# Optimization experiments

Hardware: AMD Instinct MI355X
Metric: run time of the kernel (lower is better)

Reference implementation:

```python
import jax, jax.numpy as jnp
import numpy as np

V = 100000      # item vocab
N1, N2, N3 = 100000, 20000, 5000
EMB = 128       # embedding_dim == hidden_dim
H, Dh = 8, 16   # num_heads, per-head dim (H*Dh == EMB)
NEG_SLOPE = 0.2


def setup_inputs() -> dict:
    key = jax.random.key(0)
    ks = jax.random.split(key, 32)
    ki = iter(range(32))
    def nrm(shape, scale=0.1):
        return jax.random.normal(ks[next(ki)], shape, dtype=jnp.float32) * scale
    def ridx(n, hi):
        return jax.random.randint(ks[next(ki)], (n,), 0, hi, dtype=jnp.int32)
    inp = {}
    # graph structure
    inp['item_ids'] = ridx(N1, V)
    inp['seq1_src'] = ridx(600000, N1); inp['seq1_dst'] = ridx(600000, N1)
    inp['seq2_src'] = ridx(120000, N2); inp['seq2_dst'] = ridx(120000, N2)
    inp['seq3_src'] = ridx(30000, N3);  inp['seq3_dst'] = ridx(30000, N3)
    inp['up1_src']   = ridx(200000, N1); inp['up1_dst']   = ridx(200000, N2)
    inp['down1_src'] = ridx(200000, N2); inp['down1_dst'] = ridx(200000, N1)
    inp['up2_src']   = ridx(60000, N2);  inp['up2_dst']   = ridx(60000, N3)
    inp['down2_src'] = ridx(60000, N3);  inp['down2_dst'] = ridx(60000, N2)
    # parameters: 7 GATConvs in order [seq1, seq2, seq3, up1, down1, up2, down2]
    inp['item_emb'] = nrm((V, EMB), 1.0)
    inp['fc_w']   = nrm((7, EMB, H * Dh))   # DGL fc (bias=False)
    inp['attn_l'] = nrm((7, H, Dh))
    inp['attn_r'] = nrm((7, H, Dh))
    inp['conv_b'] = nrm((7, H * Dh))        # GATConv bias
    # 3 readout MLPs: Linear(hid,hid)->ReLU->Linear(hid,emb)
    inp['r_w1'] = nrm((3, EMB, EMB)); inp['r_b1'] = nrm((3, EMB))
    inp['r_w2'] = nrm((3, EMB, EMB)); inp['r_b2'] = nrm((3, EMB))
    inp['gran_w'] = jnp.ones((3,), dtype=jnp.float32)
    return inp


def gat(h_src, h_dst, src, dst, W, al, ar, b, residual):
    """DGL GATConv (eval mode, no dropout, no activation)."""
    Ns, Nd = h_src.shape[0], h_dst.shape[0]
    fs = (h_src @ W).reshape(Ns, H, Dh)   # [Ns,H,Dh]
    fd = (h_dst @ W).reshape(Nd, H, Dh)
    el = jnp.sum(fs * al, axis=-1)        # [Ns,H]
    er = jnp.sum(fd * ar, axis=-1)        # [Nd,H]
    e = jax.nn.leaky_relu(el[src] + er[dst], NEG_SLOPE)   # [E,H]
    m = jax.ops.segment_max(e, dst, num_segments=Nd)      # edge-softmax per dst
    ez = jnp.exp(e - m[dst])
    denom = jax.ops.segment_sum(ez, dst, num_segments=Nd)
    alpha = ez / denom[dst]                                # [E,H]
    msg = alpha[:, :, None] * fs[src]                      # [E,H,Dh]
    out = jax.ops.segment_sum(msg, dst, num_segments=Nd)   # [Nd,H,Dh]
    if residual:  # in_feats == H*Dh -> identity residual
        out = out + h_dst.reshape(Nd, H, Dh)
    out = out + b.reshape(1, H, Dh)
    return out.reshape(Nd, H * Dh)


def reference(item_emb, fc_w, attn_l, attn_r, conv_b,
              r_w1, r_b1, r_w2, r_b2, gran_w,
              item_ids, seq1_src, seq1_dst, seq2_src, seq2_dst,
              seq3_src, seq3_dst, up1_src, up1_dst, down1_src, down1_dst,
              up2_src, up2_dst, down2_src, down2_dst):
    h1 = item_emb[item_ids]                           # gran_1 from embedding lookup
    h2 = jnp.zeros((N2, EMB), dtype=item_emb.dtype)   # gran_2/3 init to zeros
    h3 = jnp.zeros((N3, EMB), dtype=item_emb.dtype)
    def g(i, hs, hd, s, d, res):
        return gat(hs, hd, s, d, fc_w[i], attn_l[i], attn_r[i], conv_b[i], res)
    out1 = g(0, h1, h1, seq1_src, seq1_dst, True) + g(4, h2, h1, down1_src, down1_dst, False)
    out2 = (g(1, h2, h2, seq2_src, seq2_dst, True)
            + g(3, h1, h2, up1_src, up1_dst, False)
            + g(6, h3, h2, down2_src, down2_dst, False))
    out3 = g(2, h3, h3, seq3_src, seq3_dst, True) + g(5, h2, h3, up2_src, up2_dst, False)
    reprs = []
    for k, x in enumerate((out1, out2, out3)):
        r = jax.nn.relu(x @ r_w1[k] + r_b1[k]) @ r_w2[k] + r_b2[k]
        reprs.append(jnp.mean(r, axis=0))             # session readout mean
    stack = jnp.stack(reprs, axis=0)                  # [3, EMB]
    weights = jax.nn.softmax(gran_w)
    fused = jnp.sum(stack * weights[:, None], axis=0) # [EMB]
    return fused, stack, weights
```

## Files before the change

### kernel.cpp

```cpp
#include <hip/hip_runtime.h>
#include <math.h>

#define N1 100000
#define N2 20000
#define EMB 128
#define NH 8
#define TILE 64
#define LPAD 132

static constexpr float NEG = 0.2f;

__global__ __launch_bounds__(256) void k_feat64(
    const float* __restrict__ item_emb, const int* __restrict__ item_ids,
    const float* __restrict__ fc_w, const float* __restrict__ attn_l,
    const float* __restrict__ attn_r,
    float* __restrict__ h1, float* __restrict__ fs0, float* __restrict__ fs3,
    float* __restrict__ el0, float* __restrict__ er0, float* __restrict__ el3)
{
    __shared__ float xs[TILE][LPAD];

    const int tid = threadIdx.x;
    const int nbase = blockIdx.x * TILE;

    #pragma unroll
    for (int r = 0; r < 8; ++r) {
        int f4 = r * 256 + tid;
        int t  = f4 >> 5;
        int c4 = f4 & 31;
        int node = nbase + t;
        if (node < N1) {
            int row = item_ids[node];
            float4 v = ((const float4*)(item_emb + (size_t)row * EMB))[c4];
            ((float4*)&xs[t][0])[c4] = v;
            ((float4*)(h1 + (size_t)node * EMB))[c4] = v;
        }
    }
    __syncthreads();

    const int cg = tid & 31;
    const int rg = tid >> 5;
    const int j0 = cg * 4;
    const float* W0 = fc_w + j0;
    const float* W3 = fc_w + 3 * EMB * EMB + j0;

    float a0[8][4], a3[8][4];
    #pragma unroll
    for (int r = 0; r < 8; ++r)
        #pragma unroll
        for (int c = 0; c < 4; ++c) { a0[r][c] = 0.f; a3[r][c] = 0.f; }

    for (int k = 0; k < EMB; k += 4) {
        float w0v[4][4], w3v[4][4];
        #pragma unroll
        for (int kk = 0; kk < 4; ++kk) {
            float4 t0 = *((const float4*)(W0 + (size_t)(k + kk) * EMB));
            float4 t3 = *((const float4*)(W3 + (size_t)(k + kk) * EMB));
            w0v[kk][0] = t0.x; w0v[kk][1] = t0.y; w0v[kk][2] = t0.z; w0v[kk][3] = t0.w;
            w3v[kk][0] = t3.x; w3v[kk][1] = t3.y; w3v[kk][2] = t3.z; w3v[kk][3] = t3.w;
        }
        #pragma unroll
        for (int r = 0; r < 8; ++r) {
            float4 x = *((const float4*)&xs[rg * 8 + r][k]);
            #pragma unroll
            for (int c = 0; c < 4; ++c) {
                a0[r][c] = fmaf(x.x, w0v[0][c], a0[r][c]);
                a0[r][c] = fmaf(x.y, w0v[1][c], a0[r][c]);
                a0[r][c] = fmaf(x.z, w0v[2][c], a0[r][c]);
                a0[r][c] = fmaf(x.w, w0v[3][c], a0[r][c]);
                a3[r][c] = fmaf(x.x, w3v[0][c], a3[r][c]);
                a3[r][c] = fmaf(x.y, w3v[1][c], a3[r][c]);
                a3[r][c] = fmaf(x.z, w3v[2][c], a3[r][c]);
                a3[r][c] = fmaf(x.w, w3v[3][c], a3[r][c]);
            }
        }
    }

    #pragma unroll
    for (int r = 0; r < 8; ++r) {
        int row = nbase + rg * 8 + r;
        if (row < N1) {
            float4 v0 = make_float4(a0[r][0], a0[r][1], a0[r][2], a0[r][3]);
            float4 v3 = make_float4(a3[r][0], a3[r][1], a3[r][2], a3[r][3]);
            *((float4*)(fs0 + (size_t)row * EMB + j0)) = v0;
            *((float4*)(fs3 + (size_t)row * EMB + j0)) = v3;
        }
    }

    float al0v[4], ar0v[4], al3v[4];
    #pragma unroll
    for (int c = 0; c < 4; ++c) {
        al0v[c] = attn_l[j0 + c];
        ar0v[c] = attn_r[j0 + c];
        al3v[c] = attn_l[3 * EMB + j0 + c];
    }
    const int head = j0 >> 4;
    #pragma unroll
    for (int r = 0; r < 8; ++r) {
        float pe = a0[r][0]*al0v[0] + a0[r][1]*al0v[1] + a0[r][2]*al0v[2] + a0[r][3]*al0v[3];
        float pr = a0[r][0]*ar0v[0] + a0[r][1]*ar0v[1] + a0[r][2]*ar0v[2] + a0[r][3]*ar0v[3];
        float p3 = a3[r][0]*al3v[0] + a3[r][1]*al3v[1] + a3[r][2]*al3v[2] + a3[r][3]*al3v[3];
        pe += __shfl_xor(pe, 1); pe += __shfl_xor(pe, 2);
        pr += __shfl_xor(pr, 1); pr += __shfl_xor(pr, 2);
        p3 += __shfl_xor(p3, 1); p3 += __shfl_xor(p3, 2);
        int row = nbase + rg * 8 + r;
        if ((cg & 3) == 0 && row < N1) {
            el0[(size_t)row * NH + head] = pe;
            er0[(size_t)row * NH + head] = pr;
            el3[(size_t)row * NH + head] = p3;
        }
    }
}

__global__ __launch_bounds__(256) void k_count(
    const int* __restrict__ dst, int nE, int* __restrict__ cnt)
{
    int i = blockIdx.x * 256 + threadIdx.x;
    if (i < nE) atomicAdd(&cnt[dst[i]], 1);
}

__global__ __launch_bounds__(256) void k_scan_partial(
    const int* __restrict__ cnt, int n, int* __restrict__ part)
{
    __shared__ int sh[256];
    int base = blockIdx.x * 1024 + threadIdx.x * 4;
    int s = 0;
    #pragma unroll
    for (int k = 0; k < 4; ++k) { int i = base + k; if (i < n) s += cnt[i]; }
    sh[threadIdx.x] = s;
    __syncthreads();
    for (int off = 128; off > 0; off >>= 1) {
        if (threadIdx.x < off) sh[threadIdx.x] += sh[threadIdx.x + off];
        __syncthreads();
    }
    if (threadIdx.x == 0) part[blockIdx.x] = sh[0];
}

__global__ __launch_bounds__(256) void k_scan_mid(int* part, int np)
{
    __shared__ int sh[256];
    int tid = threadIdx.x;
    int v = (tid < np) ? part[tid] : 0;
    sh[tid] = v;
    __syncthreads();
    for (int off = 1; off < 256; off <<= 1) {
        int t = (tid >= off) ? sh[tid - off] : 0;
        __syncthreads();
        sh[tid] += t;
        __syncthreads();
    }
    if (tid < np) part[tid] = sh[tid] - v;
}

__global__ __launch_bounds__(256) void k_scan_final(
    const int* __restrict__ cnt, const int* __restrict__ part, int n, int nE,
    int* __restrict__ off, int* __restrict__ cur)
{
    __shared__ int sh[256];
    int tid = threadIdx.x;
    int base = blockIdx.x * 1024 + tid * 4;
    int c[4]; int s = 0;
    #pragma unroll
    for (int k = 0; k < 4; ++k) { int i = base + k; c[k] = (i < n) ? cnt[i] : 0; s += c[k]; }
    sh[tid] = s;
    __syncthreads();
    int own = s;
    for (int offv = 1; offv < 256; offv <<= 1) {
        int t = (tid >= offv) ? sh[tid - offv] : 0;
        __syncthreads();
        sh[tid] += t;
        __syncthreads();
    }
    int excl = sh[tid] - own + part[blockIdx.x];
    #pragma unroll
    for (int k = 0; k < 4; ++k) {
        int i = base + k;
        if (i < n) { off[i] = excl; cur[i] = excl; excl += c[k]; }
    }
    if (blockIdx.x == 0 && tid == 0) off[n] = nE;
}

__global__ __launch_bounds__(256) void k_scatter(
    const int* __restrict__ src, const int* __restrict__ dst, int nE,
    int* __restrict__ cur, int* __restrict__ esrc)
{
    int i = blockIdx.x * 256 + threadIdx.x;
    if (i < nE) {
        int pos = atomicAdd(&cur[dst[i]], 1);
        esrc[pos] = src[i];
    }
}

__global__ __launch_bounds__(256) void k_aggregate(
    const int* __restrict__ off, const int* __restrict__ esrc,
    const float* __restrict__ el, const float* __restrict__ er,
    const float* __restrict__ fs, const float* __restrict__ resid,
    const float* __restrict__ conv_b, int ia, int ib, int ic,
    float* __restrict__ val)
{
    const int d = blockIdx.x * 4 + (threadIdx.x >> 6);
    const int lane = threadIdx.x & 63;
    const int h = lane >> 3;
    const int beg = off[d], end = off[d + 1];
    const float erh = er ? er[(size_t)d * NH + h] : 0.f;

    float ax = 0.f, ay = 0.f, wsum = 0.f;
    for (int base = beg; base < end; base += 64) {
        int myS = (base + lane < end) ? esrc[base + lane] : 0;
        int cnt = min(64, end - base);
        for (int i = 0; i < cnt; ++i) {
            int s = __shfl(myS, i);
            float e = el[(size_t)s * NH + h] + erh;
            e = (e > 0.f) ? e : NEG * e;
            float w = expf(e);
            float2 f2 = ((const float2*)(fs + (size_t)s * EMB))[lane];
            ax = fmaf(w, f2.x, ax);
            ay = fmaf(w, f2.y, ay);
            wsum += w;
        }
    }

    float vx = 0.f, vy = 0.f;
    if (end > beg) { float inv = 1.f / wsum; vx = ax * inv; vy = ay * inv; }
    if (resid) {
        float2 r = ((const float2*)(resid + (size_t)d * EMB))[lane];
        vx += r.x; vy += r.y;
    }
    const int c = lane * 2;
    float b0 = conv_b[ia * EMB + c]     + conv_b[ib * EMB + c];
    float b1 = conv_b[ia * EMB + c + 1] + conv_b[ib * EMB + c + 1];
    if (ic >= 0) { b0 += conv_b[ic * EMB + c]; b1 += conv_b[ic * EMB + c + 1]; }
    float2 o; o.x = vx + b0; o.y = vy + b1;
    ((float2*)(val + (size_t)d * EMB))[lane] = o;
}

__global__ __launch_bounds__(256) void k_mlp64(
    const float* __restrict__ val, int nrows,
    const float* __restrict__ rw1, const float* __restrict__ rb1,
    float* __restrict__ mean)
{
    __shared__ float xs[TILE][LPAD];
    __shared__ float red[8][EMB];

    const int tid = threadIdx.x;
    const int nbase = blockIdx.x * TILE;

    #pragma unroll
    for (int r = 0; r < 8; ++r) {
        int f4 = r * 256 + tid;
        int t  = f4 >> 5;
        int c4 = f4 & 31;
        int row = nbase + t;
        if (row < nrows)
            ((float4*)&xs[t][0])[c4] =
                ((const float4*)(val + (size_t)row * EMB))[c4];
    }
    __syncthreads();

    const int cg = tid & 31;
    const int rg = tid >> 5;
    const int j0 = cg * 4;
    const float* W = rw1 + j0;

    float a[8][4];
    #pragma unroll
    for (int r = 0; r < 8; ++r)
        #pragma unroll
        for (int c = 0; c < 4; ++c) a[r][c] = 0.f;

    for (int k = 0; k < EMB; k += 4) {
        float wv[4][4];
        #pragma unroll
        for (int kk = 0; kk < 4; ++kk) {
            float4 t0 = *((const float4*)(W + (size_t)(k + kk) * EMB));
            wv[kk][0] = t0.x; wv[kk][1] = t0.y; wv[kk][2] = t0.z; wv[kk][3] = t0.w;
        }
        #pragma unroll
        for (int r = 0; r < 8; ++r) {
            float4 x = *((const float4*)&xs[rg * 8 + r][k]);
            #pragma unroll
            for (int c = 0; c < 4; ++c) {
                a[r][c] = fmaf(x.x, wv[0][c], a[r][c]);
                a[r][c] = fmaf(x.y, wv[1][c], a[r][c]);
                a[r][c] = fmaf(x.z, wv[2][c], a[r][c]);
                a[r][c] = fmaf(x.w, wv[3][c], a[r][c]);
            }
        }
    }

    float b1v[4];
    #pragma unroll
    for (int c = 0; c < 4; ++c) b1v[c] = rb1[j0 + c];
    float cs[4] = {0.f, 0.f, 0.f, 0.f};
    #pragma unroll
    for (int r = 0; r < 8; ++r) {
        int row = nbase + rg * 8 + r;
        if (row < nrows) {
            #pragma unroll
            for (int c = 0; c < 4; ++c)
                cs[c] += fmaxf(a[r][c] + b1v[c], 0.f);
        }
    }
    *((float4*)&red[rg][j0]) = make_float4(cs[0], cs[1], cs[2], cs[3]);
    __syncthreads();
    if (tid < EMB) {
        float s = 0.f;
        #pragma unroll
        for (int g = 0; g < 8; ++g) s += red[g][tid];
        atomicAdd(mean + tid, s);
    }
}

__global__ __launch_bounds__(128) void k_final(
    const float* __restrict__ mean1, const float* __restrict__ mean2,
    const float* __restrict__ conv_b,
    const float* __restrict__ r_w1, const float* __restrict__ r_b1,
    const float* __restrict__ r_w2, const float* __restrict__ r_b2,
    const float* __restrict__ gran_w, float* __restrict__ out)
{
    __shared__ float m1[EMB], m2[EMB], x3[EMB], t3[EMB];
    const int j = threadIdx.x;
    m1[j] = mean1[j] * (1.f / N1);
    m2[j] = mean2[j] * (1.f / N2);
    x3[j] = conv_b[2 * EMB + j] + conv_b[5 * EMB + j];
    __syncthreads();

    float a = r_b1[2 * EMB + j];
    for (int k = 0; k < EMB; ++k)
        a = fmaf(x3[k], r_w1[2 * EMB * EMB + k * EMB + j], a);
    t3[j] = fmaxf(a, 0.f);
    __syncthreads();

    float r1 = r_b2[0 * EMB + j];
    float r2 = r_b2[1 * EMB + j];
    float r3 = r_b2[2 * EMB + j];
    for (int k = 0; k < EMB; ++k) {
        r1 = fmaf(m1[k], r_w2[0 * EMB * EMB + k * EMB + j], r1);
        r2 = fmaf(m2[k], r_w2[1 * EMB * EMB + k * EMB + j], r2);
        r3 = fmaf(t3[k], r_w2[2 * EMB * EMB + k * EMB + j], r3);
    }

    float g0 = gran_w[0], g1 = gran_w[1], g2 = gran_w[2];
    float mx = fmaxf(g0, fmaxf(g1, g2));
    float e0 = expf(g0 - mx), e1 = expf(g1 - mx), e2 = expf(g2 - mx);
    float s = e0 + e1 + e2;
    float w0 = e0 / s, w1 = e1 / s, w2 = e2 / s;

    out[j]       = w0 * r1 + w1 * r2 + w2 * r3;
    out[128 + j] = r1;
    out[256 + j] = r2;
    out[384 + j] = r3;
    if (j < 3) out[512 + j] = (j == 0) ? w0 : (j == 1) ? w1 : w2;
}

extern "C" void kernel_launch(void* const* d_in, const int* in_sizes, int n_in,
                              void* d_out, int out_size, void* d_ws, size_t ws_size,
                              hipStream_t stream) {
    const int*   item_ids = (const int*)d_in[0];
    const int*   s1s = (const int*)d_in[1];
    const int*   s1d = (const int*)d_in[2];
    const int*   u1s = (const int*)d_in[7];
    const int*   u1d = (const int*)d_in[8];
    const float* item_emb = (const float*)d_in[15];
    const float* fc_w   = (const float*)d_in[16];
    const float* attn_l = (const float*)d_in[17];
    const float* attn_r = (const float*)d_in[18];
    const float* conv_b = (const float*)d_in[19];
    const float* r_w1 = (const float*)d_in[20];
    const float* r_b1 = (const float*)d_in[21];
    const float* r_w2 = (const float*)d_in[22];
    const float* r_b2 = (const float*)d_in[23];
    const float* gran_w = (const float*)d_in[24];

    const int nE1 = in_sizes[1];
    const int nE3 = in_sizes[7];

    float* ws = (float*)d_ws;
    float* mean1 = ws;
    float* mean2 = mean1 + EMB;
    int*   cnt1  = (int*)(mean2 + EMB);
    int*   cnt2  = cnt1 + N1;
    size_t zeroN = 2 * EMB + N1 + N2;
    int*   off1  = cnt2 + N2;
    int*   cur1  = off1 + N1 + 1;
    int*   off2  = cur1 + N1;
    int*   cur2  = off2 + N2 + 1;
    int*   part1 = cur2 + N2;
    int*   part2 = part1 + 128;
    int*   esrc1 = part2 + 128;
    int*   esrc2 = esrc1 + nE1;
    float* h1   = (float*)(esrc2 + nE3);
    float* fs0  = h1  + (size_t)N1 * EMB;
    float* fs3  = fs0 + (size_t)N1 * EMB;
    float* el0  = fs3 + (size_t)N1 * EMB;
    float* er0  = el0 + (size_t)N1 * NH;
    float* el3  = er0 + (size_t)N1 * NH;
    float* val1 = el3 + (size_t)N1 * NH;
    float* val2 = val1 + (size_t)N1 * EMB;

    hipMemsetAsync(ws, 0, zeroN * sizeof(float), stream);

    k_feat64<<<(N1 + TILE - 1) / TILE, 256, 0, stream>>>(
        item_emb, item_ids, fc_w, attn_l, attn_r, h1, fs0, fs3, el0, er0, el3);

    const int nch1 = (N1 + 1023) / 1024;
    k_count<<<(nE1 + 255) / 256, 256, 0, stream>>>(s1d, nE1, cnt1);
    k_scan_partial<<<nch1, 256, 0, stream>>>(cnt1, N1, part1);
    k_scan_mid<<<1, 256, 0, stream>>>(part1, nch1);
    k_scan_final<<<nch1, 256, 0, stream>>>(cnt1, part1, N1, nE1, off1, cur1);
    k_scatter<<<(nE1 + 255) / 256, 256, 0, stream>>>(s1s, s1d, nE1, cur1, esrc1);

    const int nch2 = (N2 + 1023) / 1024;
    k_count<<<(nE3 + 255) / 256, 256, 0, stream>>>(u1d, nE3, cnt2);
    k_scan_partial<<<nch2, 256, 0, stream>>>(cnt2, N2, part2);
    k_scan_mid<<<1, 256, 0, stream>>>(part2, nch2);
    k_scan_final<<<nch2, 256, 0, stream>>>(cnt2, part2, N2, nE3, off2, cur2);
    k_scatter<<<(nE3 + 255) / 256, 256, 0, stream>>>(u1s, u1d, nE3, cur2, esrc2);

    k_aggregate<<<N1 / 4, 256, 0, stream>>>(off1, esrc1, el0, er0, fs0, h1,
                                            conv_b, 0, 4, -1, val1);
    k_aggregate<<<N2 / 4, 256, 0, stream>>>(off2, esrc2, el3, nullptr, fs3, nullptr,
                                            conv_b, 3, 1, 6, val2);

    k_mlp64<<<(N1 + TILE - 1) / TILE, 256, 0, stream>>>(
        val1, N1, r_w1 + 0 * EMB * EMB, r_b1 + 0 * EMB, mean1);
    k_mlp64<<<(N2 + TILE - 1) / TILE, 256, 0, stream>>>(
        val2, N2, r_w1 + 1 * EMB * EMB, r_b1 + 1 * EMB, mean2);

    k_final<<<1, 128, 0, stream>>>(mean1, mean2, conv_b, r_w1, r_b1, r_w2, r_b2,
                                   gran_w, (float*)d_out);
}
```

Before: 585.2 us.

## Merge both graph CSR builds and aggregations into single launches, drop h1 buffer

Concatenates the seq1 and up1 edge sets so one count, scan, scatter and aggregate launch handles both destination sets, which halves the number of small kernel launches. The separate h1 copy is no longer written; the aggregate kernel reads the residual directly from the embedding table. It also adds register double-buffering of weight loads in the two GEMM kernels, unrolls the edge loop by two, and switches expf to __expf. The costs are branchier kernels and slightly lower exp precision.

```diff
diff --git a/kernel.cpp b/kernel.cpp
--- a/kernel.cpp
+++ b/kernel.cpp
@@ -10,11 +10,13 @@
 
 static constexpr float NEG = 0.2f;
 
+#define F4C(v, c) ((c) == 0 ? (v).x : (c) == 1 ? (v).y : (c) == 2 ? (v).z : (v).w)
+
 __global__ __launch_bounds__(256) void k_feat64(
     const float* __restrict__ item_emb, const int* __restrict__ item_ids,
     const float* __restrict__ fc_w, const float* __restrict__ attn_l,
     const float* __restrict__ attn_r,
-    float* __restrict__ h1, float* __restrict__ fs0, float* __restrict__ fs3,
+    float* __restrict__ fs0, float* __restrict__ fs3,
     float* __restrict__ el0, float* __restrict__ er0, float* __restrict__ el3)
 {
     __shared__ float xs[TILE][LPAD];
@@ -30,9 +32,8 @@
         int node = nbase + t;
         if (node < N1) {
             int row = item_ids[node];
-            float4 v = ((const float4*)(item_emb + (size_t)row * EMB))[c4];
-            ((float4*)&xs[t][0])[c4] = v;
-            ((float4*)(h1 + (size_t)node * EMB))[c4] = v;
+            ((float4*)&xs[t][0])[c4] =
+                ((const float4*)(item_emb + (size_t)row * EMB))[c4];
         }
     }
     __syncthreads();
@@ -49,29 +50,42 @@
         #pragma unroll
         for (int c = 0; c < 4; ++c) { a0[r][c] = 0.f; a3[r][c] = 0.f; }
 
+    float4 wc0[4], wc3[4], wn0[4], wn3[4];
+    #pragma unroll
+    for (int kk = 0; kk < 4; ++kk) {
+        wc0[kk] = *((const float4*)(W0 + (size_t)kk * EMB));
+        wc3[kk] = *((const float4*)(W3 + (size_t)kk * EMB));
+    }
+
     for (int k = 0; k < EMB; k += 4) {
-        float w0v[4][4], w3v[4][4];
-        #pragma unroll
-        for (int kk = 0; kk < 4; ++kk) {
-            float4 t0 = *((const float4*)(W0 + (size_t)(k + kk) * EMB));
-            float4 t3 = *((const float4*)(W3 + (size_t)(k + kk) * EMB));
-            w0v[kk][0] = t0.x; w0v[kk][1] = t0.y; w0v[kk][2] = t0.z; w0v[kk][3] = t0.w;
-            w3v[kk][0] = t3.x; w3v[kk][1] = t3.y; w3v[kk][2] = t3.z; w3v[kk][3] = t3.w;
+        const int kn = k + 4;
+        if (kn < EMB) {
+            #pragma unroll
+            for (int kk = 0; kk < 4; ++kk) {
+                wn0[kk] = *((const float4*)(W0 + (size_t)(kn + kk) * EMB));
+                wn3[kk] = *((const float4*)(W3 + (size_t)(kn + kk) * EMB));
+            }
         }
         #pragma unroll
         for (int r = 0; r < 8; ++r) {
             float4 x = *((const float4*)&xs[rg * 8 + r][k]);
             #pragma unroll
             for (int c = 0; c < 4; ++c) {
-                a0[r][c] = fmaf(x.x, w0v[0][c], a0[r][c]);
-                a0[r][c] = fmaf(x.y, w0v[1][c], a0[r][c]);
-                a0[r][c] = fmaf(x.z, w0v[2][c], a0[r][c]);
-                a0[r][c] = fmaf(x.w, w0v[3][c], a0[r][c]);
-                a3[r][c] = fmaf(x.x, w3v[0][c], a3[r][c]);
-                a3[r][c] = fmaf(x.y, w3v[1][c], a3[r][c]);
-                a3[r][c] = fmaf(x.z, w3v[2][c], a3[r][c]);
-                a3[r][c] = fmaf(x.w, w3v[3][c], a3[r][c]);
+                float acc0 = a0[r][c], acc3 = a3[r][c];
+                acc0 = fmaf(x.x, F4C(wc0[0], c), acc0);
+                acc0 = fmaf(x.y, F4C(wc0[1], c), acc0);
+                acc0 = fmaf(x.z, F4C(wc0[2], c), acc0);
+                acc0 = fmaf(x.w, F4C(wc0[3], c), acc0);
+                acc3 = fmaf(x.x, F4C(wc3[0], c), acc3);
+                acc3 = fmaf(x.y, F4C(wc3[1], c), acc3);
+                acc3 = fmaf(x.z, F4C(wc3[2], c), acc3);
+                acc3 = fmaf(x.w, F4C(wc3[3], c), acc3);
+                a0[r][c] = acc0; a3[r][c] = acc3;
             }
+        }
+        if (kn < EMB) {
+            #pragma unroll
+            for (int kk = 0; kk < 4; ++kk) { wc0[kk] = wn0[kk]; wc3[kk] = wn3[kk]; }
         }
     }
 
@@ -111,11 +125,13 @@
     }
 }
 
-__global__ __launch_bounds__(256) void k_count(
-    const int* __restrict__ dst, int nE, int* __restrict__ cnt)
+__global__ __launch_bounds__(256) void k_count2(
+    const int* __restrict__ s1d, int nE1,
+    const int* __restrict__ u1d, int nE3, int* __restrict__ cnt)
 {
     int i = blockIdx.x * 256 + threadIdx.x;
-    if (i < nE) atomicAdd(&cnt[dst[i]], 1);
+    if (i < nE1) atomicAdd(&cnt[s1d[i]], 1);
+    else if (i < nE1 + nE3) atomicAdd(&cnt[N1 + u1d[i - nE1]], 1);
 }
 
 __global__ __launch_bounds__(256) void k_scan_partial(
@@ -179,39 +195,77 @@
     if (blockIdx.x == 0 && tid == 0) off[n] = nE;
 }
 
-__global__ __launch_bounds__(256) void k_scatter(
-    const int* __restrict__ src, const int* __restrict__ dst, int nE,
+__global__ __launch_bounds__(256) void k_scatter2(
+    const int* __restrict__ s1s, const int* __restrict__ s1d, int nE1,
+    const int* __restrict__ u1s, const int* __restrict__ u1d, int nE3,
     int* __restrict__ cur, int* __restrict__ esrc)
 {
     int i = blockIdx.x * 256 + threadIdx.x;
-    if (i < nE) {
-        int pos = atomicAdd(&cur[dst[i]], 1);
-        esrc[pos] = src[i];
-    }
-}
-
-__global__ __launch_bounds__(256) void k_aggregate(
+    if (i < nE1) {
+        int pos = atomicAdd(&cur[s1d[i]], 1);
+        esrc[pos] = s1s[i];
+    } else if (i < nE1 + nE3) {
+        int j = i - nE1;
+        int pos = atomicAdd(&cur[N1 + u1d[j]], 1);
+        esrc[pos] = u1s[j];
+    }
+}
+
+__global__ __launch_bounds__(256) void k_agg(
     const int* __restrict__ off, const int* __restrict__ esrc,
-    const float* __restrict__ el, const float* __restrict__ er,
-    const float* __restrict__ fs, const float* __restrict__ resid,
-    const float* __restrict__ conv_b, int ia, int ib, int ic,
-    float* __restrict__ val)
-{
-    const int d = blockIdx.x * 4 + (threadIdx.x >> 6);
+    const float* __restrict__ el0, const float* __restrict__ er0,
+    const float* __restrict__ fs0,
+    const float* __restrict__ el3, const float* __restrict__ fs3,
+    const float* __restrict__ item_emb, const int* __restrict__ item_ids,
+    const float* __restrict__ conv_b,
+    float* __restrict__ val1, float* __restrict__ val2)
+{
+    const int wid  = blockIdx.x * 4 + (threadIdx.x >> 6);
     const int lane = threadIdx.x & 63;
     const int h = lane >> 3;
-    const int beg = off[d], end = off[d + 1];
-    const float erh = er ? er[(size_t)d * NH + h] : 0.f;
-
+    const int c = lane * 2;
+
+    const float* el; const float* fs;
+    float erh, b0, b1;
+    bool g1 = (wid < N1);
+    if (g1) {
+        el = el0; fs = fs0;
+        erh = er0[(size_t)wid * NH + h];
+        b0 = conv_b[0 * EMB + c]     + conv_b[4 * EMB + c];
+        b1 = conv_b[0 * EMB + c + 1] + conv_b[4 * EMB + c + 1];
+    } else {
+        el = el3; fs = fs3;
+        erh = 0.f;
+        b0 = conv_b[3 * EMB + c]     + conv_b[1 * EMB + c]     + conv_b[6 * EMB + c];
+        b1 = conv_b[3 * EMB + c + 1] + conv_b[1 * EMB + c + 1] + conv_b[6 * EMB + c + 1];
+    }
+
+    const int beg = off[wid], end = off[wid + 1];
     float ax = 0.f, ay = 0.f, wsum = 0.f;
     for (int base = beg; base < end; base += 64) {
         int myS = (base + lane < end) ? esrc[base + lane] : 0;
         int cnt = min(64, end - base);
-        for (int i = 0; i < cnt; ++i) {
+        int i = 0;
+        for (; i + 1 < cnt; i += 2) {
+            int sA = __shfl(myS, i);
+            int sB = __shfl(myS, i + 1);
+            float eA = el[(size_t)sA * NH + h] + erh;
+            float eB = el[(size_t)sB * NH + h] + erh;
+            eA = (eA > 0.f) ? eA : NEG * eA;
+            eB = (eB > 0.f) ? eB : NEG * eB;
+            float wA = __expf(eA);
+            float wB = __expf(eB);
+            float2 fA = ((const float2*)(fs + (size_t)sA * EMB))[lane];
+            float2 fB = ((const float2*)(fs + (size_t)sB * EMB))[lane];
+            ax = fmaf(wA, fA.x, fmaf(wB, fB.x, ax));
+            ay = fmaf(wA, fA.y, fmaf(wB, fB.y, ay));
+            wsum += wA + wB;
+        }
+        if (i < cnt) {
             int s = __shfl(myS, i);
             float e = el[(size_t)s * NH + h] + erh;
             e = (e > 0.f) ? e : NEG * e;
-            float w = expf(e);
+            float w = __expf(e);
             float2 f2 = ((const float2*)(fs + (size_t)s * EMB))[lane];
             ax = fmaf(w, f2.x, ax);
             ay = fmaf(w, f2.y, ay);
@@ -221,16 +275,13 @@
 
     float vx = 0.f, vy = 0.f;
     if (end > beg) { float inv = 1.f / wsum; vx = ax * inv; vy = ay * inv; }
-    if (resid) {
-        float2 r = ((const float2*)(resid + (size_t)d * EMB))[lane];
+    if (g1) {
+        float2 r = ((const float2*)(item_emb + (size_t)item_ids[wid] * EMB))[lane];
         vx += r.x; vy += r.y;
     }
-    const int c = lane * 2;
-    float b0 = conv_b[ia * EMB + c]     + conv_b[ib * EMB + c];
-    float b1 = conv_b[ia * EMB + c + 1] + conv_b[ib * EMB + c + 1];
-    if (ic >= 0) { b0 += conv_b[ic * EMB + c]; b1 += conv_b[ic * EMB + c + 1]; }
     float2 o; o.x = vx + b0; o.y = vy + b1;
-    ((float2*)(val + (size_t)d * EMB))[lane] = o;
+    float* out = g1 ? (val1 + (size_t)wid * EMB) : (val2 + (size_t)(wid - N1) * EMB);
+    ((float2*)out)[lane] = o;
 }
 
 __global__ __launch_bounds__(256) void k_mlp64(
@@ -267,23 +318,33 @@
         #pragma unroll
         for (int c = 0; c < 4; ++c) a[r][c] = 0.f;
 
+    float4 wc[4], wn[4];
+    #pragma unroll
+    for (int kk = 0; kk < 4; ++kk) wc[kk] = *((const float4*)(W + (size_t)kk * EMB));
+
     for (int k = 0; k < EMB; k += 4) {
-        float wv[4][4];
-        #pragma unroll
-        for (int kk = 0; kk < 4; ++kk) {
-            float4 t0 = *((const float4*)(W + (size_t)(k + kk) * EMB));
-            wv[kk][0] = t0.x; wv[kk][1] = t0.y; wv[kk][2] = t0.z; wv[kk][3] = t0.w;
+        const int kn = k + 4;
+        if (kn < EMB) {
+            #pragma unroll
+            for (int kk = 0; kk < 4; ++kk)
+                wn[kk] = *((const float4*)(W + (size_t)(kn + kk) * EMB));
         }
         #pragma unroll
         for (int r = 0; r < 8; ++r) {
             float4 x = *((const float4*)&xs[rg * 8 + r][k]);
             #pragma unroll
             for (int c = 0; c < 4; ++c) {
-                a[r][c] = fmaf(x.x, wv[0][c], a[r][c]);
-                a[r][c] = fmaf(x.y, wv[1][c], a[r][c]);
-                a[r][c] = fmaf(x.z, wv[2][c], a[r][c]);
-                a[r][c] = fmaf(x.w, wv[3][c], a[r][c]);
+                float acc = a[r][c];
+                acc = fmaf(x.x, F4C(wc[0], c), acc);
+                acc = fmaf(x.y, F4C(wc[1], c), acc);
+                acc = fmaf(x.z, F4C(wc[2], c), acc);
+                acc = fmaf(x.w, F4C(wc[3], c), acc);
+                a[r][c] = acc;
             }
+        }
+        if (kn < EMB) {
+            #pragma unroll
+            for (int kk = 0; kk < 4; ++kk) wc[kk] = wn[kk];
         }
     }
 
@@ -373,53 +434,41 @@
 
     const int nE1 = in_sizes[1];
     const int nE3 = in_sizes[7];
+    const int nEt = nE1 + nE3;
+    const int ND  = N1 + N2;
 
     float* ws = (float*)d_ws;
     float* mean1 = ws;
     float* mean2 = mean1 + EMB;
-    int*   cnt1  = (int*)(mean2 + EMB);
-    int*   cnt2  = cnt1 + N1;
-    size_t zeroN = 2 * EMB + N1 + N2;
-    int*   off1  = cnt2 + N2;
-    int*   cur1  = off1 + N1 + 1;
-    int*   off2  = cur1 + N1;
-    int*   cur2  = off2 + N2 + 1;
-    int*   part1 = cur2 + N2;
-    int*   part2 = part1 + 128;
-    int*   esrc1 = part2 + 128;
-    int*   esrc2 = esrc1 + nE1;
-    float* h1   = (float*)(esrc2 + nE3);
-    float* fs0  = h1  + (size_t)N1 * EMB;
-    float* fs3  = fs0 + (size_t)N1 * EMB;
-    float* el0  = fs3 + (size_t)N1 * EMB;
-    float* er0  = el0 + (size_t)N1 * NH;
-    float* el3  = er0 + (size_t)N1 * NH;
-    float* val1 = el3 + (size_t)N1 * NH;
-    float* val2 = val1 + (size_t)N1 * EMB;
+    int*   cnt   = (int*)(mean2 + EMB);
+    size_t zeroN = 2 * EMB + ND;
+    int*   off   = cnt + ND;
+    int*   cur   = off + ND + 4;
+    int*   part  = cur + ND;
+    int*   esrc  = part + 128;
+    float* fs0   = (float*)(esrc + nEt);
+    float* fs3   = fs0 + (size_t)N1 * EMB;
+    float* el0   = fs3 + (size_t)N1 * EMB;
+    float* er0   = el0 + (size_t)N1 * NH;
+    float* el3   = er0 + (size_t)N1 * NH;
+    float* val1  = el3 + (size_t)N1 * NH;
+    float* val2  = val1 + (size_t)N1 * EMB;
 
     hipMemsetAsync(ws, 0, zeroN * sizeof(float), stream);
 
     k_feat64<<<(N1 + TILE - 1) / TILE, 256, 0, stream>>>(
-        item_emb, item_ids, fc_w, attn_l, attn_r, h1, fs0, fs3, el0, er0, el3);
-
-    const int nch1 = (N1 + 1023) / 1024;
-    k_count<<<(nE1 + 255) / 256, 256, 0, stream>>>(s1d, nE1, cnt1);
-    k_scan_partial<<<nch1, 256, 0, stream>>>(cnt1, N1, part1);
-    k_scan_mid<<<1, 256, 0, stream>>>(part1, nch1);
-    k_scan_final<<<nch1, 256, 0, stream>>>(cnt1, part1, N1, nE1, off1, cur1);
-    k_scatter<<<(nE1 + 255) / 256, 256, 0, stream>>>(s1s, s1d, nE1, cur1, esrc1);
-
-    const int nch2 = (N2 + 1023) / 1024;
-    k_count<<<(nE3 + 255) / 256, 256, 0, stream>>>(u1d, nE3, cnt2);
-    k_scan_partial<<<nch2, 256, 0, stream>>>(cnt2, N2, part2);
-    k_scan_mid<<<1, 256, 0, stream>>>(part2, nch2);
-    k_scan_final<<<nch2, 256, 0, stream>>>(cnt2, part2, N2, nE3, off2, cur2);
-    k_scatter<<<(nE3 + 255) / 256, 256, 0, stream>>>(u1s, u1d, nE3, cur2, esrc2);
-
-    k_aggregate<<<N1 / 4, 256, 0, stream>>>(off1, esrc1, el0, er0, fs0, h1,
-                                            conv_b, 0, 4, -1, val1);
-    k_aggregate<<<N2 / 4, 256, 0, stream>>>(off2, esrc2, el3, nullptr, fs3, nullptr,
-                                            conv_b, 3, 1, 6, val2);
+        item_emb, item_ids, fc_w, attn_l, attn_r, fs0, fs3, el0, er0, el3);
+
+    const int nch = (ND + 1023) / 1024;
+    k_count2<<<(nEt + 255) / 256, 256, 0, stream>>>(s1d, nE1, u1d, nE3, cnt);
+    k_scan_partial<<<nch, 256, 0, stream>>>(cnt, ND, part);
+    k_scan_mid<<<1, 256, 0, stream>>>(part, nch);
+    k_scan_final<<<nch, 256, 0, stream>>>(cnt, part, ND, nEt, off, cur);
+    k_scatter2<<<(nEt + 255) / 256, 256, 0, stream>>>(s1s, s1d, nE1,
+                                                      u1s, u1d, nE3, cur, esrc);
+
+    k_agg<<<ND / 4, 256, 0, stream>>>(off, esrc, el0, er0, fs0, el3, fs3,
+                                      item_emb, item_ids, conv_b, val1, val2);
 
     k_mlp64<<<(N1 + TILE - 1) / TILE, 256, 0, stream>>>(
         val1, N1, r_w1 + 0 * EMB * EMB, r_b1 + 0 * EMB, mean1);
```

New measurement: 560.4 us. -4.2%, faster.
